# Performance work log

Hardware: AMD Instinct MI355X
Metric: run time of the kernel (lower is better)

The kernel has to match this reference:

```python
import jax, jax.numpy as jnp
import numpy as np

D_IN = 1024
D_OUT = 1024
NUM_HEADS = 16
DIM_HEAD = D_OUT // NUM_HEADS


def setup_inputs() -> dict:
    key = jax.random.key(0)
    ks = jax.random.split(key, 6)
    s = 0.02
    x = jax.random.normal(ks[0], (2, 2048, D_IN), dtype=jnp.float32)
    Wk = jax.random.normal(ks[1], (D_IN, D_OUT), dtype=jnp.float32) * s
    Wq = jax.random.normal(ks[2], (D_IN, D_OUT), dtype=jnp.float32) * s
    Wv = jax.random.normal(ks[3], (D_IN, D_OUT), dtype=jnp.float32) * s
    Wo = jax.random.normal(ks[4], (D_OUT, D_OUT), dtype=jnp.float32) * s
    bo = jax.random.normal(ks[5], (D_OUT,), dtype=jnp.float32) * s
    return {"x": x, "Wk": Wk, "Wq": Wq, "Wv": Wv, "Wo": Wo, "bo": bo}


def reference(x, Wk, Wq, Wv, Wo, bo):
    B, S, _ = x.shape
    # projections -> [B, H, S, Dh]
    def split_heads(t):
        return t.reshape(B, S, NUM_HEADS, DIM_HEAD).transpose(0, 2, 1, 3)
    q = split_heads(x @ Wq)
    k = split_heads(x @ Wk)
    v = split_heads(x @ Wv)
    # NOTE: source uses non-in-place masked_fill whose result is discarded,
    # so NO causal mask is actually applied (faithful reproduction).
    scores = jnp.einsum("bhqd,bhkd->bhqk", q, k) / jnp.sqrt(jnp.float32(DIM_HEAD))
    wgts = jax.nn.softmax(scores, axis=-1)  # dropout = identity (eval mode)
    ctx = jnp.einsum("bhqk,bhkd->bhqd", wgts, v)
    ctx = ctx.transpose(0, 2, 1, 3).reshape(B, S, D_OUT)
    return ctx @ Wo + bo
```

## Files before the change

kernel.cpp:

```cpp
#include <hip/hip_runtime.h>
#include <stdint.h>

typedef short bf16x8 __attribute__((ext_vector_type(8)));
typedef short s16x4  __attribute__((ext_vector_type(4)));
typedef float f32x4  __attribute__((ext_vector_type(4)));
typedef unsigned int u32x4 __attribute__((ext_vector_type(4)));
typedef unsigned int u32x2 __attribute__((ext_vector_type(2)));

__device__ __forceinline__ unsigned short f2bf(float f) {
  unsigned int u = __builtin_bit_cast(unsigned int, f) + 0x8000u;
  return (unsigned short)(u >> 16);
}
__device__ __forceinline__ unsigned int pack2bf(float a, float b) {
  unsigned int ua = __builtin_bit_cast(unsigned int, a) + 0x8000u;
  unsigned int ub = __builtin_bit_cast(unsigned int, b) + 0x8000u;
  return __builtin_amdgcn_perm(ub, ua, 0x07060302);
}

__device__ __forceinline__ void gl2lds16(const void* g, void* l) {
  __builtin_amdgcn_global_load_lds(
      (const __attribute__((address_space(1))) void*)g,
      (__attribute__((address_space(3))) void*)l, 16, 0, 0);
}

__global__ __launch_bounds__(256) void cast_x_k(const float* __restrict__ x,
                                                unsigned short* __restrict__ xb) {
  int i = blockIdx.x * 256 + threadIdx.x;
  float4 v = ((const float4*)x)[i];
  u32x2 o;
  o.x = pack2bf(v.x, v.y);
  o.y = pack2bf(v.z, v.w);
  ((u32x2*)xb)[i] = o;
}

__global__ __launch_bounds__(256) void castT_k(
    const float* __restrict__ Wq, const float* __restrict__ Wk,
    const float* __restrict__ Wv, const float* __restrict__ Wo,
    unsigned short* __restrict__ Tq, unsigned short* __restrict__ Tk,
    unsigned short* __restrict__ Tv, unsigned short* __restrict__ To) {
  __shared__ float tile[32][33];
  const int z = blockIdx.z;
  const float* W = (z == 0) ? Wq : (z == 1) ? Wk : (z == 2) ? Wv : Wo;
  unsigned short* T = (z == 0) ? Tq : (z == 1) ? Tk : (z == 2) ? Tv : To;
  const int tx = threadIdx.x, ty = threadIdx.y;
  const int n0 = blockIdx.x * 32, k0 = blockIdx.y * 32;
#pragma unroll
  for (int j = 0; j < 32; j += 8)
    tile[ty + j][tx] = W[(size_t)(k0 + ty + j) * 1024 + n0 + tx];
  __syncthreads();
#pragma unroll
  for (int j = 0; j < 32; j += 8)
    T[(size_t)(n0 + ty + j) * 1024 + k0 + tx] = f2bf(tile[tx][ty + j]);
}

template <int MODE, int TN>
__global__ __launch_bounds__(256) void gemm_bt_k(const unsigned short* __restrict__ A,
                                                 const unsigned short* __restrict__ B,
                                                 void* __restrict__ C,
                                                 const float* __restrict__ bias,
                                                 int K) {
  __shared__ alignas(16) short lA[1024 * 8];
  __shared__ alignas(16) short lB[256 * TN * 8];
  const int tid = threadIdx.x;
  const int wid = tid >> 6, lane = tid & 63;
  const int l15 = lane & 15, quad = lane >> 4;
  const int waveM = wid >> 1, waveN = wid & 1;
  const int bm = blockIdx.y * 128, bn = blockIdx.x * (32 * TN);

  f32x4 acc[4][TN];
#pragma unroll
  for (int i = 0; i < 4; ++i)
#pragma unroll
    for (int j = 0; j < TN; ++j) acc[i][j] = (f32x4){0.f, 0.f, 0.f, 0.f};

  for (int kk = 0; kk < K; kk += 64) {
    __syncthreads();
#pragma unroll
    for (int j = 0; j < 4; ++j) {
      int c = tid + 256 * j;
      int row = ((c >> 7) << 4) | (c & 15);
      int ch = (c >> 4) & 7;
      gl2lds16(A + (size_t)(bm + row) * K + kk + ch * 8, &lA[(c & ~63) * 8]);
    }
#pragma unroll
    for (int j = 0; j < TN; ++j) {
      int c = tid + 256 * j;
      int row = ((c >> 7) << 4) | (c & 15);
      int ch = (c >> 4) & 7;
      gl2lds16(B + (size_t)(bn + row) * K + kk + ch * 8, &lB[(c & ~63) * 8]);
    }
    __syncthreads();
#pragma unroll
    for (int ks = 0; ks < 2; ++ks) {
      bf16x8 af[4], bfr[TN];
#pragma unroll
      for (int i = 0; i < 4; ++i)
        af[i] = *(bf16x8*)&lA[(((waveM * 4 + i) * 2 + ks) * 64 + lane) * 8];
#pragma unroll
      for (int j = 0; j < TN; ++j)
        bfr[j] = *(bf16x8*)&lB[(((waveN * TN + j) * 2 + ks) * 64 + lane) * 8];
#pragma unroll
      for (int i = 0; i < 4; ++i)
#pragma unroll
        for (int j = 0; j < TN; ++j)
          acc[i][j] = __builtin_amdgcn_mfma_f32_16x16x32_bf16(af[i], bfr[j], acc[i][j], 0, 0, 0);
    }
  }

#pragma unroll
  for (int i = 0; i < 4; ++i)
#pragma unroll
    for (int j = 0; j < TN; ++j) {
      int row = bm + waveM * 64 + i * 16 + quad * 4;
      int col = bn + (waveN * TN + j) * 16 + l15;
      if (MODE == 0) {
        unsigned short* Cq = (unsigned short*)C;
        int w = col >> 10, n1 = col & 1023;
        int h = n1 >> 6, d = n1 & 63;
        int b = row >> 11, s = row & 2047;
        int bhh = (b << 4) + h;
        if (w == 2) {
          int g = (i << 2) + quad;
          int ks2 = g >> 3, rem = g & 7;
          int pos = ((ks2 << 2) + (rem & 3)) * 8 + (rem >> 2) * 4;
          u32x2 pk;
          pk.x = pack2bf(acc[i][j][0], acc[i][j][1]);
          pk.y = pack2bf(acc[i][j][2], acc[i][j][3]);
          *(u32x2*)&Cq[(size_t)2 * 4194304 + ((size_t)bhh * 64 + d) * 2048 +
                       (s & ~63) + pos] = pk;
        } else {
          float sc = (w == 0) ? 0.18033688011112042f : 1.0f;
#pragma unroll
          for (int r = 0; r < 4; ++r)
            Cq[(size_t)w * 4194304 + ((size_t)bhh * 2048 + s + r) * 64 + d] =
                f2bf(acc[i][j][r] * sc);
        }
      } else {
#pragma unroll
        for (int r = 0; r < 4; ++r)
          ((float*)C)[(size_t)(row + r) * 1024 + col] = acc[i][j][r] + bias[col];
      }
    }
}

__global__ __launch_bounds__(128) void flash_k(const unsigned short* __restrict__ Qh,
                                               const unsigned short* __restrict__ Kh,
                                               const unsigned short* __restrict__ Vt,
                                               unsigned short* __restrict__ ctxb) {
  constexpr int SL = 2048;
  __shared__ alignas(16) short kt[2][512 * 8];
  __shared__ alignas(16) short vt[2][512 * 8];

  const int tid = threadIdx.x;
  const int wid = tid >> 6, lane = tid & 63;
  const int l15 = lane & 15, quad = lane >> 4;
  const int bh = blockIdx.y;
  const int q0 = blockIdx.x * 64 + wid * 32;

  const unsigned short* Qb = Qh + (size_t)bh * SL * 64;
  const unsigned short* Kb = Kh + (size_t)bh * SL * 64;
  const unsigned short* Vb = Vt + (size_t)bh * 64 * SL;

  bf16x8 qf[2][2];
#pragma unroll
  for (int s = 0; s < 2; ++s)
#pragma unroll
    for (int ks = 0; ks < 2; ++ks)
      qf[s][ks] = *(const bf16x8*)(Qb + (size_t)(q0 + s * 16 + l15) * 64 + ks * 32 + quad * 8);

  f32x4 o[2][4];
  f32x4 rs4[2] = {(f32x4){0.f, 0.f, 0.f, 0.f}, (f32x4){0.f, 0.f, 0.f, 0.f}};
  const f32x4 z4 = (f32x4){0.f, 0.f, 0.f, 0.f};
#pragma unroll
  for (int s = 0; s < 2; ++s)
#pragma unroll
    for (int t = 0; t < 4; ++t) o[s][t] = z4;

  auto stage = [&](int kb, short* ktb, short* vtb) {
#pragma unroll
    for (int j2 = 0; j2 < 4; ++j2) {
      int cc = tid + 128 * j2;
      int row = cc >> 3;
      int ko = (cc & 7) ^ (row & 7);
      gl2lds16(Kb + (size_t)(kb + row) * 64 + ko * 8, &ktb[(cc & ~63) * 8]);
      gl2lds16(Vb + (size_t)row * SL + kb + ko * 8, &vtb[(cc & ~63) * 8]);
    }
  };

  auto compute = [&](const short* ktb, const short* vtb) {
    f32x4 sv[2][4];
#pragma unroll
    for (int t = 0; t < 4; ++t) {
      int key = t * 16 + l15;
      bf16x8 kf0 = *(bf16x8*)&ktb[(key * 8 + (quad ^ (key & 7))) * 8];
      bf16x8 kf1 = *(bf16x8*)&ktb[(key * 8 + ((4 + quad) ^ (key & 7))) * 8];
#pragma unroll
      for (int s = 0; s < 2; ++s) {
        sv[s][t] = __builtin_amdgcn_mfma_f32_16x16x32_bf16(kf0, qf[s][0], z4, 0, 0, 0);
        sv[s][t] = __builtin_amdgcn_mfma_f32_16x16x32_bf16(kf1, qf[s][1], sv[s][t], 0, 0, 0);
      }
    }
    u32x4 pf[2][2];
#pragma unroll
    for (int s = 0; s < 2; ++s)
#pragma unroll
      for (int t = 0; t < 4; ++t) {
        f32x4 p;
#pragma unroll
        for (int r = 0; r < 4; ++r) p[r] = __builtin_amdgcn_exp2f(sv[s][t][r]);
        rs4[s] += p;
        pf[s][t >> 1][(t & 1) * 2 + 0] = pack2bf(p[0], p[1]);
        pf[s][t >> 1][(t & 1) * 2 + 1] = pack2bf(p[2], p[3]);
      }
#pragma unroll
    for (int t = 0; t < 4; ++t) {
      int d = t * 16 + l15;
#pragma unroll
      for (int ks = 0; ks < 2; ++ks) {
        bf16x8 vf = *(bf16x8*)&vtb[(d * 8 + ((ks * 4 + quad) ^ (d & 7))) * 8];
#pragma unroll
        for (int s = 0; s < 2; ++s)
          o[s][t] = __builtin_amdgcn_mfma_f32_16x16x32_bf16(
              vf, __builtin_bit_cast(bf16x8, pf[s][ks]), o[s][t], 0, 0, 0);
      }
    }
  };

  stage(0, kt[0], vt[0]);
#pragma unroll 1
  for (int i2 = 0; i2 < 16; ++i2) {
    __syncthreads();
    stage((2 * i2 + 1) * 64, kt[1], vt[1]);
    compute(kt[0], vt[0]);
    __syncthreads();
    if (i2 < 15) stage((2 * i2 + 2) * 64, kt[0], vt[0]);
    compute(kt[1], vt[1]);
  }

  const int bb = bh >> 4, h = bh & 15;
#pragma unroll
  for (int s = 0; s < 2; ++s) {
    float v = (rs4[s][0] + rs4[s][1]) + (rs4[s][2] + rs4[s][3]);
    v += __shfl_xor(v, 16);
    v += __shfl_xor(v, 32);
    float inv = 1.0f / v;
    int tok = q0 + s * 16 + l15;
    size_t base = ((size_t)(bb * 2048 + tok)) * 1024 + h * 64;
#pragma unroll
    for (int t = 0; t < 4; ++t) {
      u32x2 pk;
      pk.x = pack2bf(o[s][t][0] * inv, o[s][t][1] * inv);
      pk.y = pack2bf(o[s][t][2] * inv, o[s][t][3] * inv);
      *(u32x2*)&ctxb[base + t * 16 + quad * 4] = pk;
    }
  }
}

extern "C" void kernel_launch(void* const* d_in, const int* in_sizes, int n_in,
                              void* d_out, int out_size, void* d_ws, size_t ws_size,
                              hipStream_t stream) {
  const float* x  = (const float*)d_in[0];
  const float* Wk = (const float*)d_in[1];
  const float* Wq = (const float*)d_in[2];
  const float* Wv = (const float*)d_in[3];
  const float* Wo = (const float*)d_in[4];
  const float* bo = (const float*)d_in[5];
  float* out = (float*)d_out;

  char* ws = (char*)d_ws;
  const size_t MB = 1u << 20;
  unsigned short* xb   = (unsigned short*)(ws);
  unsigned short* WqT  = (unsigned short*)(ws + 8  * MB);
  unsigned short* WkT  = (unsigned short*)(ws + 10 * MB);
  unsigned short* WvT  = (unsigned short*)(ws + 12 * MB);
  unsigned short* WoT  = (unsigned short*)(ws + 14 * MB);
  unsigned short* Qh   = (unsigned short*)(ws + 16 * MB);
  unsigned short* ctxb = xb;

  cast_x_k<<<4096, 256, 0, stream>>>(x, xb);
  castT_k<<<dim3(32, 32, 4), dim3(32, 8), 0, stream>>>(Wq, Wk, Wv, Wo, WqT, WkT, WvT, WoT);
  gemm_bt_k<0, 4><<<dim3(24, 32), 256, 0, stream>>>(xb, WqT, Qh, nullptr, 1024);
  flash_k<<<dim3(32, 32), 128, 0, stream>>>(Qh, Qh + 4194304, Qh + 2 * 4194304, ctxb);
  gemm_bt_k<1, 2><<<dim3(16, 32), 256, 0, stream>>>(ctxb, WoT, out, bo, 1024);
}
```

Baseline: 229.0 us.

## Double-buffer GEMM LDS tiles and remap blocks for XCD-aware locality

Double-buffers the A/B LDS tiles in the projection GEMMs so the global-to-LDS load of the next K-slice is issued before the MFMA work on the current slice. The grid also becomes 1D, with block IDs remapped so that consecutive tiles land on the same XCD (bid&7 interleave), which should improve L2 reuse. In exchange, LDS use per block doubles, which may lower occupancy. The loop also assumes K is a multiple of 128.

```diff
diff --git a/kernel.cpp b/kernel.cpp
--- a/kernel.cpp
+++ b/kernel.cpp
@@ -58,14 +58,16 @@
                                                  const unsigned short* __restrict__ B,
                                                  void* __restrict__ C,
                                                  const float* __restrict__ bias,
-                                                 int K) {
-  __shared__ alignas(16) short lA[1024 * 8];
-  __shared__ alignas(16) short lB[256 * TN * 8];
+                                                 int K, int nbx, int cpx) {
+  __shared__ alignas(16) short lA[2][1024 * 8];
+  __shared__ alignas(16) short lB[2][256 * TN * 8];
   const int tid = threadIdx.x;
   const int wid = tid >> 6, lane = tid & 63;
   const int l15 = lane & 15, quad = lane >> 4;
   const int waveM = wid >> 1, waveN = wid & 1;
-  const int bm = blockIdx.y * 128, bn = blockIdx.x * (32 * TN);
+  const int bid = blockIdx.x;
+  const int sid = (bid & 7) * cpx + (bid >> 3);
+  const int bm = (sid / nbx) * 128, bn = (sid % nbx) * (32 * TN);
 
   f32x4 acc[4][TN];
 #pragma unroll
@@ -73,38 +75,51 @@
 #pragma unroll
     for (int j = 0; j < TN; ++j) acc[i][j] = (f32x4){0.f, 0.f, 0.f, 0.f};
 
-  for (int kk = 0; kk < K; kk += 64) {
-    __syncthreads();
+  auto stage = [&](int kk, short* la, short* lb) {
 #pragma unroll
     for (int j = 0; j < 4; ++j) {
       int c = tid + 256 * j;
       int row = ((c >> 7) << 4) | (c & 15);
       int ch = (c >> 4) & 7;
-      gl2lds16(A + (size_t)(bm + row) * K + kk + ch * 8, &lA[(c & ~63) * 8]);
+      gl2lds16(A + (size_t)(bm + row) * K + kk + ch * 8, &la[(c & ~63) * 8]);
     }
 #pragma unroll
     for (int j = 0; j < TN; ++j) {
       int c = tid + 256 * j;
       int row = ((c >> 7) << 4) | (c & 15);
       int ch = (c >> 4) & 7;
-      gl2lds16(B + (size_t)(bn + row) * K + kk + ch * 8, &lB[(c & ~63) * 8]);
-    }
-    __syncthreads();
+      gl2lds16(B + (size_t)(bn + row) * K + kk + ch * 8, &lb[(c & ~63) * 8]);
+    }
+  };
+
+  auto compute = [&](const short* la, const short* lb) {
 #pragma unroll
     for (int ks = 0; ks < 2; ++ks) {
       bf16x8 af[4], bfr[TN];
 #pragma unroll
       for (int i = 0; i < 4; ++i)
-        af[i] = *(bf16x8*)&lA[(((waveM * 4 + i) * 2 + ks) * 64 + lane) * 8];
+        af[i] = *(const bf16x8*)&la[(((waveM * 4 + i) * 2 + ks) * 64 + lane) * 8];
 #pragma unroll
       for (int j = 0; j < TN; ++j)
-        bfr[j] = *(bf16x8*)&lB[(((waveN * TN + j) * 2 + ks) * 64 + lane) * 8];
+        bfr[j] = *(const bf16x8*)&lb[(((waveN * TN + j) * 2 + ks) * 64 + lane) * 8];
 #pragma unroll
       for (int i = 0; i < 4; ++i)
 #pragma unroll
         for (int j = 0; j < TN; ++j)
           acc[i][j] = __builtin_amdgcn_mfma_f32_16x16x32_bf16(af[i], bfr[j], acc[i][j], 0, 0, 0);
     }
+  };
+
+  stage(0, lA[0], lB[0]);
+  const int nt2 = K >> 7;
+#pragma unroll 1
+  for (int i2 = 0; i2 < nt2; ++i2) {
+    __syncthreads();
+    stage((2 * i2 + 1) * 64, lA[1], lB[1]);
+    compute(lA[0], lB[0]);
+    __syncthreads();
+    if (i2 + 1 < nt2) stage((2 * i2 + 2) * 64, lA[0], lB[0]);
+    compute(lA[1], lB[1]);
   }
 
 #pragma unroll
@@ -279,7 +294,7 @@
 
   cast_x_k<<<4096, 256, 0, stream>>>(x, xb);
   castT_k<<<dim3(32, 32, 4), dim3(32, 8), 0, stream>>>(Wq, Wk, Wv, Wo, WqT, WkT, WvT, WoT);
-  gemm_bt_k<0, 4><<<dim3(24, 32), 256, 0, stream>>>(xb, WqT, Qh, nullptr, 1024);
+  gemm_bt_k<0, 4><<<768, 256, 0, stream>>>(xb, WqT, Qh, nullptr, 1024, 24, 96);
   flash_k<<<dim3(32, 32), 128, 0, stream>>>(Qh, Qh + 4194304, Qh + 2 * 4194304, ctxb);
-  gemm_bt_k<1, 2><<<dim3(16, 32), 256, 0, stream>>>(ctxb, WoT, out, bo, 1024);
-}
+  gemm_bt_k<1, 2><<<512, 256, 0, stream>>>(ctxb, WoT, out, bo, 1024, 16, 64);
+}
```

Result: slower. 236.9 us (+3.5%).

## Triple-buffer GEMM LDS tiles with async loads and vmcnt-based waits

Applied to the files above, without the earlier changes.

Restructures the bf16 projection and output GEMM main loop into a three-stage software pipeline. Global-to-LDS loads for tile t+2 are issued while tile t is computed, and the K step is halved to 32 so three buffers fit in LDS. A partial s_waitcnt vmcnt plus a single barrier per step replace the previous load-then-sync pattern, so memory latency overlaps with MFMA work. The trade-off is half the MFMAs per barrier and more loop iterations, which adds overhead.

```diff
diff --git a/kernel.cpp b/kernel.cpp
--- a/kernel.cpp
+++ b/kernel.cpp
@@ -2,7 +2,6 @@
 #include <stdint.h>
 
 typedef short bf16x8 __attribute__((ext_vector_type(8)));
-typedef short s16x4  __attribute__((ext_vector_type(4)));
 typedef float f32x4  __attribute__((ext_vector_type(4)));
 typedef unsigned int u32x4 __attribute__((ext_vector_type(4)));
 typedef unsigned int u32x2 __attribute__((ext_vector_type(2)));
@@ -21,6 +20,10 @@
   __builtin_amdgcn_global_load_lds(
       (const __attribute__((address_space(1))) void*)g,
       (__attribute__((address_space(3))) void*)l, 16, 0, 0);
+}
+
+template <int N> __device__ __forceinline__ void wait_vmcnt() {
+  asm volatile("s_waitcnt vmcnt(%0)" ::"n"(N) : "memory");
 }
 
 __global__ __launch_bounds__(256) void cast_x_k(const float* __restrict__ x,
@@ -59,8 +62,9 @@
                                                  void* __restrict__ C,
                                                  const float* __restrict__ bias,
                                                  int K) {
-  __shared__ alignas(16) short lA[1024 * 8];
-  __shared__ alignas(16) short lB[256 * TN * 8];
+  __shared__ alignas(16) short lA[3][512 * 8];
+  __shared__ alignas(16) short lB[3][128 * TN * 8];
+  constexpr int PT = 2 + TN / 2;
   const int tid = threadIdx.x;
   const int wid = tid >> 6, lane = tid & 63;
   const int l15 = lane & 15, quad = lane >> 4;
@@ -73,39 +77,59 @@
 #pragma unroll
     for (int j = 0; j < TN; ++j) acc[i][j] = (f32x4){0.f, 0.f, 0.f, 0.f};
 
-  for (int kk = 0; kk < K; kk += 64) {
-    __syncthreads();
-#pragma unroll
-    for (int j = 0; j < 4; ++j) {
+  auto stage = [&](int kk, short* la, short* lb) {
+#pragma unroll
+    for (int j = 0; j < 2; ++j) {
       int c = tid + 256 * j;
-      int row = ((c >> 7) << 4) | (c & 15);
-      int ch = (c >> 4) & 7;
-      gl2lds16(A + (size_t)(bm + row) * K + kk + ch * 8, &lA[(c & ~63) * 8]);
-    }
-#pragma unroll
-    for (int j = 0; j < TN; ++j) {
+      int row = ((c >> 6) << 4) | (c & 15);
+      int ch = (c >> 4) & 3;
+      gl2lds16(A + (size_t)(bm + row) * K + kk + ch * 8, &la[(c & ~63) * 8]);
+    }
+#pragma unroll
+    for (int j = 0; j < TN / 2; ++j) {
       int c = tid + 256 * j;
-      int row = ((c >> 7) << 4) | (c & 15);
-      int ch = (c >> 4) & 7;
-      gl2lds16(B + (size_t)(bn + row) * K + kk + ch * 8, &lB[(c & ~63) * 8]);
-    }
-    __syncthreads();
-#pragma unroll
-    for (int ks = 0; ks < 2; ++ks) {
-      bf16x8 af[4], bfr[TN];
-#pragma unroll
-      for (int i = 0; i < 4; ++i)
-        af[i] = *(bf16x8*)&lA[(((waveM * 4 + i) * 2 + ks) * 64 + lane) * 8];
+      int row = ((c >> 6) << 4) | (c & 15);
+      int ch = (c >> 4) & 3;
+      gl2lds16(B + (size_t)(bn + row) * K + kk + ch * 8, &lb[(c & ~63) * 8]);
+    }
+  };
+
+  auto compute = [&](const short* la, const short* lb) {
+    bf16x8 af[4], bfr[TN];
+#pragma unroll
+    for (int i = 0; i < 4; ++i)
+      af[i] = *(const bf16x8*)&la[(((waveM * 4 + i) * 64) + lane) * 8];
+#pragma unroll
+    for (int j = 0; j < TN; ++j)
+      bfr[j] = *(const bf16x8*)&lb[(((waveN * TN + j) * 64) + lane) * 8];
+#pragma unroll
+    for (int i = 0; i < 4; ++i)
 #pragma unroll
       for (int j = 0; j < TN; ++j)
-        bfr[j] = *(bf16x8*)&lB[(((waveN * TN + j) * 2 + ks) * 64 + lane) * 8];
-#pragma unroll
-      for (int i = 0; i < 4; ++i)
-#pragma unroll
-        for (int j = 0; j < TN; ++j)
-          acc[i][j] = __builtin_amdgcn_mfma_f32_16x16x32_bf16(af[i], bfr[j], acc[i][j], 0, 0, 0);
-    }
+        acc[i][j] = __builtin_amdgcn_mfma_f32_16x16x32_bf16(af[i], bfr[j], acc[i][j], 0, 0, 0);
+  };
+
+  const int NT = K >> 5;
+  short *pa0 = lA[0], *pa1 = lA[1], *pa2 = lA[2];
+  short *pb0 = lB[0], *pb1 = lB[1], *pb2 = lB[2];
+  stage(0, pa0, pb0);
+  stage(32, pa1, pb1);
+#pragma unroll 1
+  for (int t = 0; t < NT - 1; ++t) {
+    wait_vmcnt<PT>();
+    __builtin_amdgcn_sched_barrier(0);
+    __builtin_amdgcn_s_barrier();
+    __builtin_amdgcn_sched_barrier(0);
+    if (t + 2 < NT) stage((t + 2) * 32, pa2, pb2);
+    compute(pa0, pb0);
+    short* ta = pa0; pa0 = pa1; pa1 = pa2; pa2 = ta;
+    short* tb = pb0; pb0 = pb1; pb1 = pb2; pb2 = tb;
   }
+  wait_vmcnt<0>();
+  __builtin_amdgcn_sched_barrier(0);
+  __builtin_amdgcn_s_barrier();
+  __builtin_amdgcn_sched_barrier(0);
+  compute(pa0, pb0);
 
 #pragma unroll
   for (int i = 0; i < 4; ++i)
```

New measurement: 221.0 us. -3.5%, faster.
